# Kernel optimization log

Measured on AMD Instinct MI355X. Metric: run time of the kernel, lower is better.

## Reference

```python
import jax, jax.numpy as jnp
import numpy as np

T_THRESH = 1.0  # t_thresh init arg


def _step_fn(x):
    # Heaviside forward (gradient handled separately in bwd module)
    return (x > 0).astype(x.dtype)


def setup_inputs() -> dict:
    key = jax.random.key(0)
    k1, = jax.random.split(key, 1)
    x = jax.random.normal(k1, (64, 500, 1024), dtype=jnp.float32)
    w_input = jnp.asarray(1.0, dtype=jnp.float32)
    w_leak = jnp.asarray(0.1, dtype=jnp.float32)
    return {"x": x, "w_input": w_input, "w_leak": w_leak}


def reference(x, w_input, w_leak):
    # Leaky integrate-and-fire over time axis (axis=1).
    # Vm_t = relu(w_i * x_t + (1 - w_l) * Vm_{t-1} * step(t_thresh - Vm_{t-1}))
    # spike_t = step(Vm_t - t_thresh)
    def step(Vm, xt):  # Vm, xt: [B, C]
        forget = _step_fn(T_THRESH - Vm)  # reset if Vm crossed threshold
        Vm = jax.nn.relu(w_input * xt + (1.0 - w_leak) * Vm * forget)
        spike = _step_fn(Vm - T_THRESH)
        return Vm, spike

    Vm0 = jnp.zeros_like(x[:, 0])  # [B, C]
    xt = jnp.swapaxes(x, 0, 1)  # [T, B, C]
    _, spikes = jax.lax.scan(step, Vm0, xt)
    return jnp.swapaxes(spikes, 0, 1)  # [B, T, C]
```

## Files before the change

kernel.cpp:

```cpp
#include <hip/hip_runtime.h>


#define LIF_B 64
#define LIF_T 500
#define LIF_C 1024
#define LIF_TC 20
#define LIF_NCH 25
#define LIF_NBUF 7

typedef float vfloat4 __attribute__((ext_vector_type(4)));

#define GLOBAL_AS(p) ((__attribute__((address_space(1))) const void*)(uintptr_t)(p))
#define LDS_AS(p)    ((__attribute__((address_space(3))) void*)(uintptr_t)(p))

#define VMWAIT(n) asm volatile("s_waitcnt vmcnt(" #n ")" ::: "memory")

__global__ __launch_bounds__(256) void lif_kernel(
    const float* __restrict__ x,
    const float* __restrict__ w_input_p,
    const float* __restrict__ w_leak_p,
    float* __restrict__ out) {

  __shared__ __align__(16) float lds_x[LIF_NBUF][4][LIF_TC * 64];
  __shared__ __align__(16) float sp[4][4 * 64];

  const int b     = blockIdx.x >> 2;
  const int cbase = (blockIdx.x & 3) << 8;
  const int tidx  = threadIdx.x;
  const int w     = tidx >> 6;
  const int lane  = tidx & 63;

  const float wi = w_input_p[0];
  const float kl = __fsub_rn(1.0f, w_leak_p[0]);
  asm volatile("s_waitcnt vmcnt(0) lgkmcnt(0)" ::: "memory");

  const float* xblk = x   + (size_t)b * LIF_T * LIF_C + cbase;
  float*       oblk = out + (size_t)b * LIF_T * LIF_C + cbase;

  auto stage = [&](int k, int p) {
    const float* src0 = xblk + (size_t)k * LIF_TC * LIF_C
                      + (w << 6) + ((lane & 15) << 2);
#pragma unroll
    for (int r0 = 0; r0 < LIF_TC; r0 += 4) {
      const float* g = src0 + (size_t)(r0 + (lane >> 4)) * LIF_C;
      float* l = &lds_x[p][w][r0 * 64];
      __builtin_amdgcn_global_load_lds(GLOBAL_AS(g), LDS_AS(l), 16, 0, 0);
    }
    __builtin_amdgcn_sched_barrier(0);
  };

  float Vm = 0.0f;

  auto compute = [&](int k, int p) {
    float* obase = oblk + (size_t)k * LIF_TC * LIF_C + (w << 6);
#pragma unroll
    for (int r0 = 0; r0 < LIF_TC; r0 += 4) {
#pragma unroll
      for (int dr = 0; dr < 4; ++dr) {
        const float xt  = lds_x[p][w][(r0 + dr) * 64 + lane];
        const float acc = (Vm < 1.0f) ? __fmul_rn(kl, Vm) : 0.0f;
        const float v   = __fadd_rn(__fmul_rn(wi, xt), acc);
        Vm = fmaxf(v, 0.0f);
        sp[w][dr * 64 + lane] = (Vm > 1.0f) ? 1.0f : 0.0f;
      }
      const vfloat4 v4 =
          *reinterpret_cast<const vfloat4*>(&sp[w][lane << 2]);
      float* gdst = obase + (size_t)(r0 + (lane >> 4)) * LIF_C
                  + ((lane & 15) << 2);
      __builtin_nontemporal_store(v4, reinterpret_cast<vfloat4*>(gdst));
    }
    __builtin_amdgcn_sched_barrier(0);
  };

  stage(0, 0); stage(1, 1); stage(2, 2);
  stage(3, 3); stage(4, 4); stage(5, 5);

  VMWAIT(25);
  stage(6, 6);
  compute(0, 0);

  {
    int ps = 6, pc = 0;
    for (int k = 1; k <= 18; ++k) {
      VMWAIT(30);
      if (++ps == LIF_NBUF) ps = 0;
      stage(k + 6, ps);
      if (++pc == LIF_NBUF) pc = 0;
      compute(k, pc);
    }
  }

  VMWAIT(30); compute(19, 5);
  VMWAIT(25); compute(20, 6);
  VMWAIT(20); compute(21, 0);
  VMWAIT(15); compute(22, 1);
  VMWAIT(10); compute(23, 2);
  VMWAIT(5);  compute(24, 3);
}

extern "C" void kernel_launch(void* const* d_in, const int* in_sizes, int n_in,
                              void* d_out, int out_size, void* d_ws, size_t ws_size,
                              hipStream_t stream) {
  const float* x  = (const float*)d_in[0];
  const float* wi = (const float*)d_in[1];
  const float* wl = (const float*)d_in[2];
  float* out = (float*)d_out;

  const int grid = LIF_B * (LIF_C / 256);
  lif_kernel<<<grid, 256, 0, stream>>>(x, wi, wl, out);
}
```

Baseline: 235.3 us.

## Split time axis into segments chained across blocks via global flags

Adds a new kernel in which each block owns a full batch row of 1024 channels and handles every fourth 20-step time segment. The block waits on a global flag for the previous segment's final membrane state and publishes its own state through workspace memory. This changes the per-block work from a channel slice over all 500 steps to interleaved time segments chained across the 4 blocks of a batch. The intent is wider, vectorized per-thread loads and stores (float4 per thread across the full row) and a different access pattern. It adds spin-wait latency, a memset launch, and a dependency chain that serializes the segments, with a risk of deadlock if blocks are not co-resident.

```diff
diff --git a/kernel.cpp b/kernel.cpp
--- a/kernel.cpp
+++ b/kernel.cpp
@@ -4,9 +4,11 @@
 #define LIF_B 64
 #define LIF_T 500
 #define LIF_C 1024
-#define LIF_TC 20
-#define LIF_NCH 25
-#define LIF_NBUF 7
+
+#define SEG_ROWS 20
+#define NSEG 25
+#define HALF 10
+#define NBUF 3
 
 typedef float vfloat4 __attribute__((ext_vector_type(4)));
 
@@ -15,13 +17,119 @@
 
 #define VMWAIT(n) asm volatile("s_waitcnt vmcnt(" #n ")" ::: "memory")
 
-__global__ __launch_bounds__(256) void lif_kernel(
+#define WS_VM_OFF 8192
+#define WS_NEED (WS_VM_OFF + (size_t)LIF_B * NSEG * LIF_C * 4)
+
+__global__ __launch_bounds__(256) void lif_seg_kernel(
+    const float* __restrict__ x,
+    const float* __restrict__ w_input_p,
+    const float* __restrict__ w_leak_p,
+    float* __restrict__ out,
+    int* __restrict__ flags,
+    float* __restrict__ vmbuf) {
+
+  __shared__ __align__(16) float lds[NBUF][HALF * LIF_C];
+
+  const int b    = blockIdx.x >> 2;
+  const int q    = blockIdx.x & 3;
+  const int tidx = threadIdx.x;
+  const int w    = tidx >> 6;
+  const int lane = tidx & 63;
+
+  const float wi = w_input_p[0];
+  const float kl = __fsub_rn(1.0f, w_leak_p[0]);
+
+  const float* xb  = x   + (size_t)b * LIF_T * LIF_C;
+  float*       ob  = out + (size_t)b * LIF_T * LIF_C;
+  int*         flg = flags + b * NSEG;
+  float*       vmb = vmbuf + (size_t)b * NSEG * LIF_C;
+
+  const int nseg = (q == 0) ? 7 : 6;
+  const int J    = 2 * nseg;
+
+  auto stage = [&](int j, int p) {
+    const int s  = q + 4 * (j >> 1);
+    const int t0 = SEG_ROWS * s + HALF * (j & 1);
+    const float* src0 = xb + (size_t)t0 * LIF_C + (w << 8) + (lane << 2);
+#pragma unroll
+    for (int rr = 0; rr < HALF; ++rr) {
+      __builtin_amdgcn_global_load_lds(
+          GLOBAL_AS(src0 + (size_t)rr * LIF_C),
+          LDS_AS(&lds[p][rr * LIF_C + (w << 8)]), 16, 0, 0);
+    }
+    __builtin_amdgcn_sched_barrier(0);
+  };
+
+  vfloat4 Vm4 = {0.f, 0.f, 0.f, 0.f};
+
+  stage(0, 0); stage(1, 1);
+
+  for (int j = 0; j < J; ++j) {
+    const int p3 = j % 3;
+    __syncthreads();
+    if (j + 2 < J) stage(j + 2, (j + 2) % 3);
+    const int s = q + 4 * (j >> 1);
+
+    if ((j & 1) == 0 && s > 0) {
+      const int* f = &flg[s - 1];
+      while (__hip_atomic_load(f, __ATOMIC_RELAXED,
+                               __HIP_MEMORY_SCOPE_AGENT) == 0)
+        __builtin_amdgcn_s_sleep(2);
+      (void)__hip_atomic_load(f, __ATOMIC_ACQUIRE, __HIP_MEMORY_SCOPE_AGENT);
+      const float* vsrc = &vmb[(size_t)(s - 1) * LIF_C + (tidx << 2)];
+#pragma unroll
+      for (int e = 0; e < 4; ++e)
+        Vm4[e] = __hip_atomic_load(vsrc + e, __ATOMIC_RELAXED,
+                                   __HIP_MEMORY_SCOPE_AGENT);
+    }
+
+    {
+      const int t0 = SEG_ROWS * s + HALF * (j & 1);
+      float* obase = ob + (size_t)t0 * LIF_C + (tidx << 2);
+#pragma unroll
+      for (int rr = 0; rr < HALF; ++rr) {
+        const vfloat4 xt = *reinterpret_cast<const vfloat4*>(
+            &lds[p3][rr * LIF_C + (tidx << 2)]);
+        vfloat4 spk;
+#pragma unroll
+        for (int e = 0; e < 4; ++e) {
+          float vm = Vm4[e];
+          const float acc = (vm < 1.0f) ? __fmul_rn(kl, vm) : 0.0f;
+          const float v   = __fadd_rn(__fmul_rn(wi, xt[e]), acc);
+          vm = fmaxf(v, 0.0f);
+          spk[e] = (vm > 1.0f) ? 1.0f : 0.0f;
+          Vm4[e] = vm;
+        }
+        __builtin_nontemporal_store(
+            spk, reinterpret_cast<vfloat4*>(obase + (size_t)rr * LIF_C));
+      }
+    }
+
+    if ((j & 1) == 1 && s != NSEG - 1) {
+      float* vdst = &vmb[(size_t)s * LIF_C + (tidx << 2)];
+#pragma unroll
+      for (int e = 0; e < 4; ++e)
+        __hip_atomic_store(vdst + e, Vm4[e], __ATOMIC_RELAXED,
+                           __HIP_MEMORY_SCOPE_AGENT);
+      __syncthreads();
+      if (tidx == 0)
+        __hip_atomic_store(&flg[s], 1, __ATOMIC_RELEASE,
+                           __HIP_MEMORY_SCOPE_AGENT);
+    }
+  }
+}
+
+#define R8TC 20
+#define R8NCH 25
+#define R8NBUF 7
+
+__global__ __launch_bounds__(256) void lif_kernel_r8(
     const float* __restrict__ x,
     const float* __restrict__ w_input_p,
     const float* __restrict__ w_leak_p,
     float* __restrict__ out) {
 
-  __shared__ __align__(16) float lds_x[LIF_NBUF][4][LIF_TC * 64];
+  __shared__ __align__(16) float lds_x[R8NBUF][4][R8TC * 64];
   __shared__ __align__(16) float sp[4][4 * 64];
 
   const int b     = blockIdx.x >> 2;
@@ -38,10 +146,10 @@
   float*       oblk = out + (size_t)b * LIF_T * LIF_C + cbase;
 
   auto stage = [&](int k, int p) {
-    const float* src0 = xblk + (size_t)k * LIF_TC * LIF_C
+    const float* src0 = xblk + (size_t)k * R8TC * LIF_C
                       + (w << 6) + ((lane & 15) << 2);
 #pragma unroll
-    for (int r0 = 0; r0 < LIF_TC; r0 += 4) {
+    for (int r0 = 0; r0 < R8TC; r0 += 4) {
       const float* g = src0 + (size_t)(r0 + (lane >> 4)) * LIF_C;
       float* l = &lds_x[p][w][r0 * 64];
       __builtin_amdgcn_global_load_lds(GLOBAL_AS(g), LDS_AS(l), 16, 0, 0);
@@ -52,9 +160,9 @@
   float Vm = 0.0f;
 
   auto compute = [&](int k, int p) {
-    float* obase = oblk + (size_t)k * LIF_TC * LIF_C + (w << 6);
-#pragma unroll
-    for (int r0 = 0; r0 < LIF_TC; r0 += 4) {
+    float* obase = oblk + (size_t)k * R8TC * LIF_C + (w << 6);
+#pragma unroll
+    for (int r0 = 0; r0 < R8TC; r0 += 4) {
 #pragma unroll
       for (int dr = 0; dr < 4; ++dr) {
         const float xt  = lds_x[p][w][(r0 + dr) * 64 + lane];
@@ -63,8 +171,7 @@
         Vm = fmaxf(v, 0.0f);
         sp[w][dr * 64 + lane] = (Vm > 1.0f) ? 1.0f : 0.0f;
       }
-      const vfloat4 v4 =
-          *reinterpret_cast<const vfloat4*>(&sp[w][lane << 2]);
+      const vfloat4 v4 = *reinterpret_cast<const vfloat4*>(&sp[w][lane << 2]);
       float* gdst = obase + (size_t)(r0 + (lane >> 4)) * LIF_C
                   + ((lane & 15) << 2);
       __builtin_nontemporal_store(v4, reinterpret_cast<vfloat4*>(gdst));
@@ -83,9 +190,9 @@
     int ps = 6, pc = 0;
     for (int k = 1; k <= 18; ++k) {
       VMWAIT(30);
-      if (++ps == LIF_NBUF) ps = 0;
+      if (++ps == R8NBUF) ps = 0;
       stage(k + 6, ps);
-      if (++pc == LIF_NBUF) pc = 0;
+      if (++pc == R8NBUF) pc = 0;
       compute(k, pc);
     }
   }
@@ -106,6 +213,12 @@
   const float* wl = (const float*)d_in[2];
   float* out = (float*)d_out;
 
-  const int grid = LIF_B * (LIF_C / 256);
-  lif_kernel<<<grid, 256, 0, stream>>>(x, wi, wl, out);
+  if (d_ws != nullptr && ws_size >= WS_NEED) {
+    hipMemsetAsync(d_ws, 0, WS_VM_OFF, stream);
+    int*   flags = (int*)d_ws;
+    float* vmbuf = (float*)((char*)d_ws + WS_VM_OFF);
+    lif_seg_kernel<<<LIF_B * 4, 256, 0, stream>>>(x, wi, wl, out, flags, vmbuf);
+  } else {
+    lif_kernel_r8<<<LIF_B * 4, 256, 0, stream>>>(x, wi, wl, out);
+  }
 }
```

Measured after the change: 391.7 us. 66.5% more time.
